# Kernel tuning notes

Measured on AMD Instinct MI355X. Metric: run time of the kernel, lower is better.

Reference implementation:

```python
import jax, jax.numpy as jnp
import numpy as np

NU, NI, E, D = 100000, 50000, 600000, 128
NEG_SLOPE = 0.2
EPS = 1e-12


def setup_inputs() -> dict:
    key = jax.random.key(0)
    ks = jax.random.split(key, 10)
    s = 1.0 / np.sqrt(D)  # xavier-ish scale for W
    return {
        "feat_user": jax.random.normal(ks[0], (NU, D), jnp.float32),
        "feat_item": jax.random.normal(ks[1], (NI, D), jnp.float32),
        "norm_user": jax.random.uniform(ks[2], (NU, 1), jnp.float32),
        "norm_item": jax.random.uniform(ks[3], (NI, 1), jnp.float32),
        "norm_ui": jax.random.uniform(ks[4], (E, 1), jnp.float32),
        "norm_iu": jax.random.uniform(ks[5], (E, 1), jnp.float32),
        "W1": jax.random.normal(ks[6], (D, D), jnp.float32) * s,
        "b1": jnp.zeros((D,), jnp.float32),
        "W2": jax.random.normal(ks[7], (D, D), jnp.float32) * s,
        "b2": jnp.zeros((D,), jnp.float32),
        "edge_u": jax.random.randint(ks[8], (E,), 0, NU),
        "edge_i": jax.random.randint(ks[9], (E,), 0, NI),
    }


def _post(h):
    # leaky_relu(0.2) -> dropout (eval: identity) -> row-wise L2 normalize
    h = jnp.where(h > 0, h, NEG_SLOPE * h)
    nrm = jnp.sqrt(jnp.sum(h * h, axis=1, keepdims=True))
    return h / jnp.maximum(nrm, EPS)


def reference(feat_user, feat_item, norm_user, norm_item, norm_ui, norm_iu,
              W1, b1, W2, b2, edge_u, edge_i):
    # edge_message = u_mul_v over ui edges of normed features  [E, D]
    edge_message = (feat_user * norm_user)[edge_u] * (feat_item * norm_item)[edge_i]

    # u_mul_e_sum(iu_g, feat_item, norm_iu): sum_e feat_item[i_e]*norm_iu[e] -> user
    agg_user = jax.ops.segment_sum(feat_item[edge_i] * norm_iu, edge_u, num_segments=NU)
    # u_mul_e_sum(ui_g, feat_user, norm_ui): sum_e feat_user[u_e]*norm_ui[e] -> item
    agg_item = jax.ops.segment_sum(feat_user[edge_u] * norm_ui, edge_i, num_segments=NI)

    # copy_e_sum of edge_message into user (iu dst) and item (ui dst)
    msg_user = jax.ops.segment_sum(edge_message, edge_u, num_segments=NU)
    msg_item = jax.ops.segment_sum(edge_message, edge_i, num_segments=NI)

    h_user = (feat_user + agg_user) @ W1.T + b1 + msg_user @ W2.T + b2
    h_item = (feat_item + agg_item) @ W1.T + b1 + msg_item @ W2.T + b2

    return _post(h_user), _post(h_item)
```

## Files before the change

kernel.cpp:

```cpp
#include <hip/hip_runtime.h>
#include <hip/hip_fp16.h>

#define NU_ 100000
#define NI_ 50000
#define E_  600000
#define DD  128
#define NT_ (NU_ + NI_)

#define BKN 64
#define NBKT ((NT_ + 63) >> 6)
#define SBLK 8192
#define NSB ((E_ + SBLK - 1) / SBLK)
#define NL (NBKT * NSB)
#define NSCB ((NL + 2047) / 2048)
#define MAXE 1024

#define TOBF_BLKS ((NT_ * DD / 8 + 511) / 512)
#define PACK_BLKS 8
#define PREP_BLKS (NSB + TOBF_BLKS + PACK_BLKS)

typedef short bf16x8 __attribute__((ext_vector_type(8)));
typedef float f32x4 __attribute__((ext_vector_type(4)));
typedef unsigned short u16x8 __attribute__((ext_vector_type(8)));

__device__ __forceinline__ unsigned short f2bf(float x) {
  unsigned u = __float_as_uint(x);
  return (unsigned short)((u + 0x7FFFu + ((u >> 16) & 1u)) >> 16);
}
__device__ __forceinline__ float bf2f(unsigned short h) {
  return __uint_as_float((unsigned)h << 16);
}

__device__ __forceinline__ int sidx(int L) {
  int bkt = L / NSB;
  int sb = L - bkt * NSB;
  return sb * NBKT + bkt;
}

__device__ __forceinline__ int swz(int nn, int b) {
  return nn * 256 + (b ^ ((nn & 7) << 4));
}
__device__ __forceinline__ int swz2(int row, int b) {
  return row * 512 + (b ^ ((row & 7) << 4));
}

__global__ __launch_bounds__(512) void prep_kernel(
    const float* __restrict__ fu, const float* __restrict__ fi,
    const float* __restrict__ W1, const float* __restrict__ W2,
    const int* __restrict__ eu, const int* __restrict__ ei,
    unsigned short* __restrict__ fub, unsigned short* __restrict__ fib,
    unsigned short* __restrict__ Bp, int* __restrict__ hist) {
  __shared__ int cnt[NBKT];
  int bid = blockIdx.x, tid = threadIdx.x;

  if (bid < NSB) {
    int sb = bid;
    for (int k = tid; k < NBKT; k += 512) cnt[k] = 0;
    __syncthreads();
#pragma unroll
    for (int j = 0; j < SBLK / 512; j++) {
      int e = sb * SBLK + j * 512 + tid;
      if (e < E_) {
        atomicAdd(&cnt[eu[e] >> 6], 1);
        atomicAdd(&cnt[(NU_ + ei[e]) >> 6], 1);
      }
    }
    __syncthreads();
    for (int k = tid; k < NBKT; k += 512) hist[sb * NBKT + k] = cnt[k];
    return;
  }

  if (bid < NSB + TOBF_BLKS) {
    int t = (bid - NSB) * 512 + tid;
    int nu8 = NU_ * DD / 8;
    int nt8 = NT_ * DD / 8;
    if (t >= nt8) return;
    const float* src;
    unsigned short* dst;
    int k;
    if (t < nu8) { src = fu; dst = fub; k = t; }
    else { src = fi; dst = fib; k = t - nu8; }
    const float4 v0 = reinterpret_cast<const float4*>(src)[k * 2];
    const float4 v1 = reinterpret_cast<const float4*>(src)[k * 2 + 1];
    u16x8 o;
    o[0] = f2bf(v0.x); o[1] = f2bf(v0.y); o[2] = f2bf(v0.z); o[3] = f2bf(v0.w);
    o[4] = f2bf(v1.x); o[5] = f2bf(v1.y); o[6] = f2bf(v1.z); o[7] = f2bf(v1.w);
    reinterpret_cast<u16x8*>(dst)[k] = o;
    return;
  }

  int t = (bid - NSB - TOBF_BLKS) * 512 + tid;
  if (t >= 4096) return;
  int w = t >> 11;
  int l = t & 63;
  int kt = (t >> 6) & 3;
  int nt = (t >> 8) & 7;
  const float* W = w ? W2 : W1;
  int n = nt * 16 + (l & 15);
  int k0 = kt * 32 + (l >> 4) * 8;
  unsigned short* dst = Bp + (size_t)t * 8;
#pragma unroll
  for (int j = 0; j < 8; j++) dst[j] = f2bf(W[n * DD + k0 + j]);
}

__global__ __launch_bounds__(256) void scanA_kernel(
    const int* __restrict__ hist, int* __restrict__ off, int* __restrict__ bsum) {
  __shared__ int ts[256];
  int tid = threadIdx.x;
  int base = blockIdx.x * 2048 + tid * 8;
  int v[8];
  int s = 0;
#pragma unroll
  for (int j = 0; j < 8; j++) {
    v[j] = s;
    int L = base + j;
    s += (L < NL) ? hist[sidx(L)] : 0;
  }
  ts[tid] = s;
  __syncthreads();
  for (int ofs = 1; ofs < 256; ofs <<= 1) {
    int add = (tid >= ofs) ? ts[tid - ofs] : 0;
    __syncthreads();
    ts[tid] += add;
    __syncthreads();
  }
  int texcl = ts[tid] - s;
#pragma unroll
  for (int j = 0; j < 8; j++) {
    int L = base + j;
    if (L < NL) off[sidx(L)] = texcl + v[j];
  }
  if (tid == 255) bsum[blockIdx.x] = ts[255];
}

__global__ void scanB_kernel(int* __restrict__ bsum) {
  if (threadIdx.x == 0) {
    int s = 0;
    for (int n = 0; n < NSCB; n++) {
      int t = bsum[n];
      bsum[n] = s;
      s += t;
    }
  }
}

__global__ __launch_bounds__(512) void scatter_kernel(
    const int* __restrict__ eu, const int* __restrict__ ei,
    const float* __restrict__ nui, const float* __restrict__ niu,
    const int* __restrict__ off, const int* __restrict__ bsum,
    int2* __restrict__ binned) {
  __shared__ int cur[NBKT];
  int sb = blockIdx.x, tid = threadIdx.x;
  for (int k = tid; k < NBKT; k += 512)
    cur[k] = off[sb * NBKT + k] + bsum[(k * NSB + sb) >> 11];
  __syncthreads();
#pragma unroll
  for (int j = 0; j < SBLK / 512; j++) {
    int e = sb * SBLK + j * 512 + tid;
    if (e < E_) {
      int u = eu[e], i = ei[e];
      int gi = NU_ + i;
      int s1 = atomicAdd(&cur[u >> 6], 1);
      binned[s1] = make_int2(((u & 63) << 20) | i, __float_as_int(niu[e]));
      int s2 = atomicAdd(&cur[gi >> 6], 1);
      binned[s2] = make_int2(((gi & 63) << 20) | u, __float_as_int(nui[e]));
    }
  }
}

__global__ __launch_bounds__(512, 8) void fused_kernel(
    const unsigned short* __restrict__ fub, const unsigned short* __restrict__ fib,
    const float* __restrict__ nu, const float* __restrict__ ni,
    const int* __restrict__ off, const int* __restrict__ bsum,
    const int2* __restrict__ binned,
    const unsigned short* __restrict__ Bp,
    const float* __restrict__ b1, const float* __restrict__ b2,
    float* __restrict__ out) {
  __shared__ __align__(16) unsigned short XM[2 * BKN * 128];
  __shared__ int eidx[MAXE];
  __shared__ unsigned short ew[MAXE];
  __shared__ int csrtmp[128];
  __shared__ int nstart[BKN + 1];

  unsigned short* Xs = XM;
  unsigned short* Ms = XM + BKN * 128;
  int* ncnt = csrtmp;
  int* ncur = csrtmp + 64;

  int bkt = blockIdx.x, tid = threadIdx.x;
  int bs = off[bkt] + bsum[(bkt * NSB) >> 11];
  int be = (bkt + 1 < NBKT) ? off[bkt + 1] + bsum[((bkt + 1) * NSB) >> 11] : 2 * E_;
  int cnt = be - bs;
  if (cnt > MAXE) cnt = MAXE;

  if (tid < BKN) ncnt[tid] = 0;
  __syncthreads();
  int2 e0, e1;
  bool h0 = tid < cnt, h1 = tid + 512 < cnt;
  if (h0) {
    e0 = binned[bs + tid];
    atomicAdd(&ncnt[(e0.x >> 20) & 63], 1);
  }
  if (h1) {
    e1 = binned[bs + tid + 512];
    atomicAdd(&ncnt[(e1.x >> 20) & 63], 1);
  }
  __syncthreads();

  if (tid < BKN) {
    int a = ncnt[tid];
    int incl = a;
#pragma unroll
    for (int ofs = 1; ofs < 64; ofs <<= 1) {
      int t = __shfl_up(incl, ofs);
      if (tid >= ofs) incl += t;
    }
    if (tid == 0) nstart[0] = 0;
    nstart[tid + 1] = incl;
    ncur[tid] = incl - a;
  }
  __syncthreads();

  if (h0) {
    int slot = atomicAdd(&ncur[(e0.x >> 20) & 63], 1);
    eidx[slot] = e0.x;
    ew[slot] = __half_as_ushort(__float2half(__int_as_float(e0.y)));
  }
  if (h1) {
    int slot = atomicAdd(&ncur[(e1.x >> 20) & 63], 1);
    eidx[slot] = e1.x;
    ew[slot] = __half_as_ushort(__float2half(__int_as_float(e1.y)));
  }
  __syncthreads();

  int wid = tid >> 6, lane = tid & 63;
  int q = lane >> 4, sub = lane & 15;

  for (int nn = 0; nn < 8; nn++) {
    int gl = wid * 8 + nn;
    int g = bkt * BKN + gl;
    if (g >= NT_) break;
    bool isU = g < NU_;
    const unsigned short* nbF = isU ? fib : fub;
    const float* nbS = isU ? ni : nu;
    int cs = nstart[gl], ce = nstart[gl + 1];

    float aA[8] = {0.f, 0.f, 0.f, 0.f, 0.f, 0.f, 0.f, 0.f};
    float aM[8] = {0.f, 0.f, 0.f, 0.f, 0.f, 0.f, 0.f, 0.f};
    for (int j = cs + q; j < ce; j += 4) {
      int idx = eidx[j] & 0xFFFFF;
      float w = __half2float(__ushort_as_half(ew[j]));
      float snb = nbS[idx];
      u16x8 f = *reinterpret_cast<const u16x8*>(nbF + (size_t)idx * DD + sub * 8);
#pragma unroll
      for (int d = 0; d < 8; d++) {
        float r = bf2f((unsigned short)f[d]);
        aA[d] += r * w;
        aM[d] += r * snb;
      }
    }
#pragma unroll
    for (int d = 0; d < 8; d++) {
      aA[d] += __shfl_xor(aA[d], 16);
      aA[d] += __shfl_xor(aA[d], 32);
      aM[d] += __shfl_xor(aM[d], 16);
      aM[d] += __shfl_xor(aM[d], 32);
    }

    int lrow = isU ? g : g - NU_;
    if (q < 2) {
      const unsigned short* ownp = (isU ? fub : fib) + (size_t)lrow * DD + sub * 8;
      u16x8 fo = *reinterpret_cast<const u16x8*>(ownp);
      u16x8 o;
      if (q == 0) {
#pragma unroll
        for (int d = 0; d < 8; d++)
          o[d] = f2bf(bf2f((unsigned short)fo[d]) + aA[d]);
        *reinterpret_cast<u16x8*>((char*)Xs + swz(gl, sub * 16)) = o;
      } else {
        float so = isU ? nu[lrow] : ni[lrow];
#pragma unroll
        for (int d = 0; d < 8; d++)
          o[d] = f2bf(bf2f((unsigned short)fo[d]) * so * aM[d]);
        *reinterpret_cast<u16x8*>((char*)Ms + swz(gl, sub * 16)) = o;
      }
    }
  }
  __syncthreads();

  int t = wid >> 1, colHalf = wid & 1;
  int gt0 = bkt * BKN + t * 16;
  bool active = gt0 < NT_;

  int lm = lane & 15, lh = lane >> 4;
  float h[4][4];
  float inv4[4];
  float (*ssx)[2] = (float(*)[2])csrtmp;

  if (active) {
    f32x4 acc[4];
#pragma unroll
    for (int nt = 0; nt < 4; nt++) acc[nt] = (f32x4){0.f, 0.f, 0.f, 0.f};

#pragma unroll
    for (int kt = 0; kt < 4; kt++) {
      int b = kt * 64 + lh * 16;
      bf16x8 a1 = *reinterpret_cast<const bf16x8*>((char*)Xs + swz(t * 16 + lm, b));
      bf16x8 a2 = *reinterpret_cast<const bf16x8*>((char*)Ms + swz(t * 16 + lm, b));
#pragma unroll
      for (int nt = 0; nt < 4; nt++) {
        int ntp = colHalf * 4 + nt;
        bf16x8 bf1 = *reinterpret_cast<const bf16x8*>(Bp + ((size_t)((0 * 8 + ntp) * 4 + kt) * 64 + lane) * 8);
        acc[nt] = __builtin_amdgcn_mfma_f32_16x16x32_bf16(a1, bf1, acc[nt], 0, 0, 0);
        bf16x8 bf2 = *reinterpret_cast<const bf16x8*>(Bp + ((size_t)((1 * 8 + ntp) * 4 + kt) * 64 + lane) * 8);
        acc[nt] = __builtin_amdgcn_mfma_f32_16x16x32_bf16(a2, bf2, acc[nt], 0, 0, 0);
      }
    }

    float ss[4] = {0.f, 0.f, 0.f, 0.f};
#pragma unroll
    for (int nt = 0; nt < 4; nt++) {
      int ntp = colHalf * 4 + nt;
      float bb = b1[ntp * 16 + lm] + b2[ntp * 16 + lm];
#pragma unroll
      for (int r = 0; r < 4; r++) {
        float v = acc[nt][r] + bb;
        v = (v > 0.f) ? v : 0.2f * v;
        h[nt][r] = v;
        ss[r] += v * v;
      }
    }
#pragma unroll
    for (int r = 0; r < 4; r++) {
#pragma unroll
      for (int m = 1; m < 16; m <<= 1) ss[r] += __shfl_xor(ss[r], m);
    }
    if (lm == 0) {
#pragma unroll
      for (int r = 0; r < 4; r++) ssx[t * 16 + lh * 4 + r][colHalf] = ss[r];
    }
  }
  __syncthreads();

  if (active) {
#pragma unroll
    for (int r = 0; r < 4; r++) {
      int row = t * 16 + lh * 4 + r;
      float tot = ssx[row][0] + ssx[row][1];
      inv4[r] = 1.0f / fmaxf(sqrtf(tot), 1e-12f);
    }
    float* stg = reinterpret_cast<float*>(XM);
#pragma unroll
    for (int nt = 0; nt < 4; nt++) {
      int ntp = colHalf * 4 + nt;
#pragma unroll
      for (int r = 0; r < 4; r++) {
        int row = t * 16 + lh * 4 + r;
        *reinterpret_cast<float*>((char*)stg + swz2(row, ntp * 64 + lm * 4)) =
            h[nt][r] * inv4[r];
      }
    }
  }
  __syncthreads();

  float* stg = reinterpret_cast<float*>(XM);
  int maxrow = NT_ - bkt * BKN;
  float* ob = out + (size_t)bkt * BKN * DD;
#pragma unroll
  for (int k = 0; k < 4; k++) {
    int c = k * 512 + tid;
    int row = c >> 5;
    if (row < maxrow) {
      f32x4 v = *reinterpret_cast<const f32x4*>((char*)stg + swz2(row, (c & 31) * 16));
      *reinterpret_cast<f32x4*>(ob + (size_t)c * 4) = v;
    }
  }
}

extern "C" void kernel_launch(void* const* d_in, const int* in_sizes, int n_in,
                              void* d_out, int out_size, void* d_ws, size_t ws_size,
                              hipStream_t stream) {
  const float* fu  = (const float*)d_in[0];
  const float* fi  = (const float*)d_in[1];
  const float* nu  = (const float*)d_in[2];
  const float* ni  = (const float*)d_in[3];
  const float* nui = (const float*)d_in[4];
  const float* niu = (const float*)d_in[5];
  const float* W1  = (const float*)d_in[6];
  const float* b1  = (const float*)d_in[7];
  const float* W2  = (const float*)d_in[8];
  const float* b2  = (const float*)d_in[9];
  const int* eu    = (const int*)d_in[10];
  const int* ei    = (const int*)d_in[11];
  float* out = (float*)d_out;
  char* ws = (char*)d_ws;

  size_t off_b = 0;
  auto alloc = [&](size_t bytes) {
    char* p = ws + off_b;
    off_b += (bytes + 255) & ~(size_t)255;
    return p;
  };
  unsigned short* fub = (unsigned short*)alloc((size_t)NU_ * DD * 2);
  unsigned short* fib = (unsigned short*)alloc((size_t)NI_ * DD * 2);
  unsigned short* Bp  = (unsigned short*)alloc(4096 * 8 * 2);
  int* hist = (int*)alloc((size_t)NL * 4);
  int* offc = (int*)alloc((size_t)NL * 4);
  int* bsum = (int*)alloc(256 * 4);
  int2* binned = (int2*)alloc((size_t)2 * E_ * 8);

  prep_kernel<<<PREP_BLKS, 512, 0, stream>>>(fu, fi, W1, W2, eu, ei,
                                             fub, fib, Bp, hist);
  scanA_kernel<<<NSCB, 256, 0, stream>>>(hist, offc, bsum);
  scanB_kernel<<<1, 64, 0, stream>>>(bsum);
  scatter_kernel<<<NSB, 512, 0, stream>>>(eu, ei, nui, niu, offc, bsum, binned);

  fused_kernel<<<NBKT, 512, 0, stream>>>(
      fub, fib, nu, ni, offc, bsum, binned, Bp, b1, b2, out);
}
```

Before: 166.1 us.

## Replace per-superblock histogram scan with global bucket counts and atomic cursor scatter

The binning pipeline changes from a full superblock-by-bucket histogram with a two-level scan to global bucket counts built with atomics. A single-block scan then produces bucket offsets, and the scatter claims per-block ranges through atomic global cursors. This drops one kernel launch and the large histogram traffic, and the bf16 feature conversion moves into the scatter launch. The gather loop in the fused kernel is also unrolled by two with packed float2 bf16 unpacking. Ordering of edges within a bucket becomes nondeterministic, which changes summation order.

```diff
diff --git a/kernel.cpp b/kernel.cpp
--- a/kernel.cpp
+++ b/kernel.cpp
@@ -11,16 +11,14 @@
 #define NBKT ((NT_ + 63) >> 6)
 #define SBLK 8192
 #define NSB ((E_ + SBLK - 1) / SBLK)
-#define NL (NBKT * NSB)
-#define NSCB ((NL + 2047) / 2048)
 #define MAXE 1024
 
 #define TOBF_BLKS ((NT_ * DD / 8 + 511) / 512)
 #define PACK_BLKS 8
-#define PREP_BLKS (NSB + TOBF_BLKS + PACK_BLKS)
 
 typedef short bf16x8 __attribute__((ext_vector_type(8)));
 typedef float f32x4 __attribute__((ext_vector_type(4)));
+typedef float f32x2 __attribute__((ext_vector_type(2)));
 typedef unsigned short u16x8 __attribute__((ext_vector_type(8)));
 
 __device__ __forceinline__ unsigned short f2bf(float x) {
@@ -31,12 +29,6 @@
   return __uint_as_float((unsigned)h << 16);
 }
 
-__device__ __forceinline__ int sidx(int L) {
-  int bkt = L / NSB;
-  int sb = L - bkt * NSB;
-  return sb * NBKT + bkt;
-}
-
 __device__ __forceinline__ int swz(int nn, int b) {
   return nn * 256 + (b ^ ((nn & 7) << 4));
 }
@@ -45,51 +37,33 @@
 }
 
 __global__ __launch_bounds__(512) void prep_kernel(
-    const float* __restrict__ fu, const float* __restrict__ fi,
+    const int* __restrict__ eu, const int* __restrict__ ei,
     const float* __restrict__ W1, const float* __restrict__ W2,
-    const int* __restrict__ eu, const int* __restrict__ ei,
-    unsigned short* __restrict__ fub, unsigned short* __restrict__ fib,
-    unsigned short* __restrict__ Bp, int* __restrict__ hist) {
-  __shared__ int cnt[NBKT];
+    unsigned short* __restrict__ Bp, int* __restrict__ cnt) {
+  __shared__ int loc[NBKT];
   int bid = blockIdx.x, tid = threadIdx.x;
 
   if (bid < NSB) {
     int sb = bid;
-    for (int k = tid; k < NBKT; k += 512) cnt[k] = 0;
+    for (int k = tid; k < NBKT; k += 512) loc[k] = 0;
     __syncthreads();
 #pragma unroll
     for (int j = 0; j < SBLK / 512; j++) {
       int e = sb * SBLK + j * 512 + tid;
       if (e < E_) {
-        atomicAdd(&cnt[eu[e] >> 6], 1);
-        atomicAdd(&cnt[(NU_ + ei[e]) >> 6], 1);
-      }
-    }
-    __syncthreads();
-    for (int k = tid; k < NBKT; k += 512) hist[sb * NBKT + k] = cnt[k];
+        atomicAdd(&loc[eu[e] >> 6], 1);
+        atomicAdd(&loc[(NU_ + ei[e]) >> 6], 1);
+      }
+    }
+    __syncthreads();
+    for (int k = tid; k < NBKT; k += 512) {
+      int c = loc[k];
+      if (c) atomicAdd(&cnt[k], c);
+    }
     return;
   }
 
-  if (bid < NSB + TOBF_BLKS) {
-    int t = (bid - NSB) * 512 + tid;
-    int nu8 = NU_ * DD / 8;
-    int nt8 = NT_ * DD / 8;
-    if (t >= nt8) return;
-    const float* src;
-    unsigned short* dst;
-    int k;
-    if (t < nu8) { src = fu; dst = fub; k = t; }
-    else { src = fi; dst = fib; k = t - nu8; }
-    const float4 v0 = reinterpret_cast<const float4*>(src)[k * 2];
-    const float4 v1 = reinterpret_cast<const float4*>(src)[k * 2 + 1];
-    u16x8 o;
-    o[0] = f2bf(v0.x); o[1] = f2bf(v0.y); o[2] = f2bf(v0.z); o[3] = f2bf(v0.w);
-    o[4] = f2bf(v1.x); o[5] = f2bf(v1.y); o[6] = f2bf(v1.z); o[7] = f2bf(v1.w);
-    reinterpret_cast<u16x8*>(dst)[k] = o;
-    return;
-  }
-
-  int t = (bid - NSB - TOBF_BLKS) * 512 + tid;
+  int t = (bid - NSB) * 512 + tid;
   if (t >= 4096) return;
   int w = t >> 11;
   int l = t & 63;
@@ -103,22 +77,22 @@
   for (int j = 0; j < 8; j++) dst[j] = f2bf(W[n * DD + k0 + j]);
 }
 
-__global__ __launch_bounds__(256) void scanA_kernel(
-    const int* __restrict__ hist, int* __restrict__ off, int* __restrict__ bsum) {
-  __shared__ int ts[256];
+__global__ __launch_bounds__(1024) void bscan_kernel(
+    const int* __restrict__ cnt, int* __restrict__ boff, int* __restrict__ gcur) {
+  __shared__ int ts[1024];
   int tid = threadIdx.x;
-  int base = blockIdx.x * 2048 + tid * 8;
-  int v[8];
+  int base = tid * 3;
+  int v[3];
   int s = 0;
 #pragma unroll
-  for (int j = 0; j < 8; j++) {
+  for (int j = 0; j < 3; j++) {
     v[j] = s;
-    int L = base + j;
-    s += (L < NL) ? hist[sidx(L)] : 0;
+    int k = base + j;
+    s += (k < NBKT) ? cnt[k] : 0;
   }
   ts[tid] = s;
   __syncthreads();
-  for (int ofs = 1; ofs < 256; ofs <<= 1) {
+  for (int ofs = 1; ofs < 1024; ofs <<= 1) {
     int add = (tid >= ofs) ? ts[tid - ofs] : 0;
     __syncthreads();
     ts[tid] += add;
@@ -126,53 +100,80 @@
   }
   int texcl = ts[tid] - s;
 #pragma unroll
-  for (int j = 0; j < 8; j++) {
-    int L = base + j;
-    if (L < NL) off[sidx(L)] = texcl + v[j];
-  }
-  if (tid == 255) bsum[blockIdx.x] = ts[255];
-}
-
-__global__ void scanB_kernel(int* __restrict__ bsum) {
-  if (threadIdx.x == 0) {
-    int s = 0;
-    for (int n = 0; n < NSCB; n++) {
-      int t = bsum[n];
-      bsum[n] = s;
-      s += t;
-    }
-  }
-}
-
-__global__ __launch_bounds__(512) void scatter_kernel(
+  for (int j = 0; j < 3; j++) {
+    int k = base + j;
+    if (k < NBKT) {
+      int o = texcl + v[j];
+      boff[k] = o;
+      gcur[k] = o;
+    }
+  }
+  if (tid == 1023) boff[NBKT] = ts[1023];
+}
+
+__global__ __launch_bounds__(512) void sct_kernel(
     const int* __restrict__ eu, const int* __restrict__ ei,
     const float* __restrict__ nui, const float* __restrict__ niu,
-    const int* __restrict__ off, const int* __restrict__ bsum,
-    int2* __restrict__ binned) {
-  __shared__ int cur[NBKT];
-  int sb = blockIdx.x, tid = threadIdx.x;
-  for (int k = tid; k < NBKT; k += 512)
-    cur[k] = off[sb * NBKT + k] + bsum[(k * NSB + sb) >> 11];
-  __syncthreads();
-#pragma unroll
-  for (int j = 0; j < SBLK / 512; j++) {
-    int e = sb * SBLK + j * 512 + tid;
-    if (e < E_) {
-      int u = eu[e], i = ei[e];
-      int gi = NU_ + i;
-      int s1 = atomicAdd(&cur[u >> 6], 1);
-      binned[s1] = make_int2(((u & 63) << 20) | i, __float_as_int(niu[e]));
-      int s2 = atomicAdd(&cur[gi >> 6], 1);
-      binned[s2] = make_int2(((gi & 63) << 20) | u, __float_as_int(nui[e]));
-    }
-  }
+    const float* __restrict__ fu, const float* __restrict__ fi,
+    unsigned short* __restrict__ fub, unsigned short* __restrict__ fib,
+    int* __restrict__ gcur, int2* __restrict__ binned) {
+  __shared__ int loc[NBKT];
+  int bid = blockIdx.x, tid = threadIdx.x;
+
+  if (bid < NSB) {
+    int sb = bid;
+    for (int k = tid; k < NBKT; k += 512) loc[k] = 0;
+    __syncthreads();
+#pragma unroll
+    for (int j = 0; j < SBLK / 512; j++) {
+      int e = sb * SBLK + j * 512 + tid;
+      if (e < E_) {
+        atomicAdd(&loc[eu[e] >> 6], 1);
+        atomicAdd(&loc[(NU_ + ei[e]) >> 6], 1);
+      }
+    }
+    __syncthreads();
+    for (int k = tid; k < NBKT; k += 512) {
+      int c = loc[k];
+      loc[k] = c ? atomicAdd(&gcur[k], c) : 0;
+    }
+    __syncthreads();
+#pragma unroll
+    for (int j = 0; j < SBLK / 512; j++) {
+      int e = sb * SBLK + j * 512 + tid;
+      if (e < E_) {
+        int u = eu[e], i = ei[e];
+        int gi = NU_ + i;
+        int s1 = atomicAdd(&loc[u >> 6], 1);
+        binned[s1] = make_int2(((u & 63) << 20) | i, __float_as_int(niu[e]));
+        int s2 = atomicAdd(&loc[gi >> 6], 1);
+        binned[s2] = make_int2(((gi & 63) << 20) | u, __float_as_int(nui[e]));
+      }
+    }
+    return;
+  }
+
+  int t = (bid - NSB) * 512 + tid;
+  int nu8 = NU_ * DD / 8;
+  int nt8 = NT_ * DD / 8;
+  if (t >= nt8) return;
+  const float* src;
+  unsigned short* dst;
+  int k;
+  if (t < nu8) { src = fu; dst = fub; k = t; }
+  else { src = fi; dst = fib; k = t - nu8; }
+  const float4 v0 = reinterpret_cast<const float4*>(src)[k * 2];
+  const float4 v1 = reinterpret_cast<const float4*>(src)[k * 2 + 1];
+  u16x8 o;
+  o[0] = f2bf(v0.x); o[1] = f2bf(v0.y); o[2] = f2bf(v0.z); o[3] = f2bf(v0.w);
+  o[4] = f2bf(v1.x); o[5] = f2bf(v1.y); o[6] = f2bf(v1.z); o[7] = f2bf(v1.w);
+  reinterpret_cast<u16x8*>(dst)[k] = o;
 }
 
 __global__ __launch_bounds__(512, 8) void fused_kernel(
     const unsigned short* __restrict__ fub, const unsigned short* __restrict__ fib,
     const float* __restrict__ nu, const float* __restrict__ ni,
-    const int* __restrict__ off, const int* __restrict__ bsum,
-    const int2* __restrict__ binned,
+    const int* __restrict__ boff, const int2* __restrict__ binned,
     const unsigned short* __restrict__ Bp,
     const float* __restrict__ b1, const float* __restrict__ b2,
     float* __restrict__ out) {
@@ -188,8 +189,8 @@
   int* ncur = csrtmp + 64;
 
   int bkt = blockIdx.x, tid = threadIdx.x;
-  int bs = off[bkt] + bsum[(bkt * NSB) >> 11];
-  int be = (bkt + 1 < NBKT) ? off[bkt + 1] + bsum[((bkt + 1) * NSB) >> 11] : 2 * E_;
+  int bs = boff[bkt];
+  int be = boff[bkt + 1];
   int cnt = be - bs;
   if (cnt > MAXE) cnt = MAXE;
 
@@ -223,12 +224,12 @@
 
   if (h0) {
     int slot = atomicAdd(&ncur[(e0.x >> 20) & 63], 1);
-    eidx[slot] = e0.x;
+    eidx[slot] = e0.x & 0xFFFFF;
     ew[slot] = __half_as_ushort(__float2half(__int_as_float(e0.y)));
   }
   if (h1) {
     int slot = atomicAdd(&ncur[(e1.x >> 20) & 63], 1);
-    eidx[slot] = e1.x;
+    eidx[slot] = e1.x & 0xFFFFF;
     ew[slot] = __half_as_ushort(__float2half(__int_as_float(e1.y)));
   }
   __syncthreads();
@@ -245,26 +246,59 @@
     const float* nbS = isU ? ni : nu;
     int cs = nstart[gl], ce = nstart[gl + 1];
 
-    float aA[8] = {0.f, 0.f, 0.f, 0.f, 0.f, 0.f, 0.f, 0.f};
-    float aM[8] = {0.f, 0.f, 0.f, 0.f, 0.f, 0.f, 0.f, 0.f};
-    for (int j = cs + q; j < ce; j += 4) {
-      int idx = eidx[j] & 0xFFFFF;
-      float w = __half2float(__ushort_as_half(ew[j]));
-      float snb = nbS[idx];
-      u16x8 f = *reinterpret_cast<const u16x8*>(nbF + (size_t)idx * DD + sub * 8);
-#pragma unroll
-      for (int d = 0; d < 8; d++) {
-        float r = bf2f((unsigned short)f[d]);
-        aA[d] += r * w;
-        aM[d] += r * snb;
-      }
-    }
-#pragma unroll
-    for (int d = 0; d < 8; d++) {
-      aA[d] += __shfl_xor(aA[d], 16);
-      aA[d] += __shfl_xor(aA[d], 32);
-      aM[d] += __shfl_xor(aM[d], 16);
-      aM[d] += __shfl_xor(aM[d], 32);
+    f32x2 pA[4], pM[4];
+#pragma unroll
+    for (int k = 0; k < 4; k++) {
+      pA[k] = (f32x2){0.f, 0.f};
+      pM[k] = (f32x2){0.f, 0.f};
+    }
+
+#define GPAIRS(dd, wv, sv)                                                   \
+    {                                                                        \
+      f32x2 r0, r1, r2, r3;                                                  \
+      r0.x = __uint_as_float((dd).x << 16);                                  \
+      r0.y = __uint_as_float((dd).x & 0xFFFF0000u);                          \
+      r1.x = __uint_as_float((dd).y << 16);                                  \
+      r1.y = __uint_as_float((dd).y & 0xFFFF0000u);                          \
+      r2.x = __uint_as_float((dd).z << 16);                                  \
+      r2.y = __uint_as_float((dd).z & 0xFFFF0000u);                          \
+      r3.x = __uint_as_float((dd).w << 16);                                  \
+      r3.y = __uint_as_float((dd).w & 0xFFFF0000u);                          \
+      pA[0] += r0 * (wv); pM[0] += r0 * (sv);                                \
+      pA[1] += r1 * (wv); pM[1] += r1 * (sv);                                \
+      pA[2] += r2 * (wv); pM[2] += r2 * (sv);                                \
+      pA[3] += r3 * (wv); pM[3] += r3 * (sv);                                \
+    }
+
+    int j = cs + q;
+    for (; j + 4 < ce; j += 8) {
+      int i0 = eidx[j], i1 = eidx[j + 4];
+      float w0 = __half2float(__ushort_as_half(ew[j]));
+      float w1 = __half2float(__ushort_as_half(ew[j + 4]));
+      float s0 = nbS[i0], s1 = nbS[i1];
+      uint4 d0 = *reinterpret_cast<const uint4*>(nbF + (size_t)i0 * DD + sub * 8);
+      uint4 d1 = *reinterpret_cast<const uint4*>(nbF + (size_t)i1 * DD + sub * 8);
+      f32x2 wv0 = {w0, w0}, sv0 = {s0, s0};
+      f32x2 wv1 = {w1, w1}, sv1 = {s1, s1};
+      GPAIRS(d0, wv0, sv0);
+      GPAIRS(d1, wv1, sv1);
+    }
+    if (j < ce) {
+      int i0 = eidx[j];
+      float w0 = __half2float(__ushort_as_half(ew[j]));
+      float s0 = nbS[i0];
+      uint4 d0 = *reinterpret_cast<const uint4*>(nbF + (size_t)i0 * DD + sub * 8);
+      f32x2 wv0 = {w0, w0}, sv0 = {s0, s0};
+      GPAIRS(d0, wv0, sv0);
+    }
+#undef GPAIRS
+
+#pragma unroll
+    for (int k = 0; k < 4; k++) {
+      pA[k].x += __shfl_xor(pA[k].x, 16); pA[k].x += __shfl_xor(pA[k].x, 32);
+      pA[k].y += __shfl_xor(pA[k].y, 16); pA[k].y += __shfl_xor(pA[k].y, 32);
+      pM[k].x += __shfl_xor(pM[k].x, 16); pM[k].x += __shfl_xor(pM[k].x, 32);
+      pM[k].y += __shfl_xor(pM[k].y, 16); pM[k].y += __shfl_xor(pM[k].y, 32);
     }
 
     int lrow = isU ? g : g - NU_;
@@ -274,14 +308,18 @@
       u16x8 o;
       if (q == 0) {
 #pragma unroll
-        for (int d = 0; d < 8; d++)
-          o[d] = f2bf(bf2f((unsigned short)fo[d]) + aA[d]);
+        for (int k = 0; k < 4; k++) {
+          o[2 * k] = f2bf(bf2f((unsigned short)fo[2 * k]) + pA[k].x);
+          o[2 * k + 1] = f2bf(bf2f((unsigned short)fo[2 * k + 1]) + pA[k].y);
+        }
         *reinterpret_cast<u16x8*>((char*)Xs + swz(gl, sub * 16)) = o;
       } else {
         float so = isU ? nu[lrow] : ni[lrow];
 #pragma unroll
-        for (int d = 0; d < 8; d++)
-          o[d] = f2bf(bf2f((unsigned short)fo[d]) * so * aM[d]);
+        for (int k = 0; k < 4; k++) {
+          o[2 * k] = f2bf(bf2f((unsigned short)fo[2 * k]) * so * pM[k].x);
+          o[2 * k + 1] = f2bf(bf2f((unsigned short)fo[2 * k + 1]) * so * pM[k].y);
+        }
         *reinterpret_cast<u16x8*>((char*)Ms + swz(gl, sub * 16)) = o;
       }
     }
@@ -404,17 +442,18 @@
   unsigned short* fub = (unsigned short*)alloc((size_t)NU_ * DD * 2);
   unsigned short* fib = (unsigned short*)alloc((size_t)NI_ * DD * 2);
   unsigned short* Bp  = (unsigned short*)alloc(4096 * 8 * 2);
-  int* hist = (int*)alloc((size_t)NL * 4);
-  int* offc = (int*)alloc((size_t)NL * 4);
-  int* bsum = (int*)alloc(256 * 4);
+  int* cnt  = (int*)alloc(NBKT * 4);
+  int* boff = (int*)alloc((NBKT + 1) * 4);
+  int* gcur = (int*)alloc(NBKT * 4);
   int2* binned = (int2*)alloc((size_t)2 * E_ * 8);
 
-  prep_kernel<<<PREP_BLKS, 512, 0, stream>>>(fu, fi, W1, W2, eu, ei,
-                                             fub, fib, Bp, hist);
-  scanA_kernel<<<NSCB, 256, 0, stream>>>(hist, offc, bsum);
-  scanB_kernel<<<1, 64, 0, stream>>>(bsum);
-  scatter_kernel<<<NSB, 512, 0, stream>>>(eu, ei, nui, niu, offc, bsum, binned);
+  hipMemsetAsync(cnt, 0, NBKT * sizeof(int), stream);
+
+  prep_kernel<<<NSB + PACK_BLKS, 512, 0, stream>>>(eu, ei, W1, W2, Bp, cnt);
+  bscan_kernel<<<1, 1024, 0, stream>>>(cnt, boff, gcur);
+  sct_kernel<<<NSB + TOBF_BLKS, 512, 0, stream>>>(
+      eu, ei, nui, niu, fu, fi, fub, fib, gcur, binned);
 
   fused_kernel<<<NBKT, 512, 0, stream>>>(
-      fub, fib, nu, ni, offc, bsum, binned, Bp, b1, b2, out);
-}
+      fub, fib, nu, ni, boff, binned, Bp, b1, b2, out);
+}
```

Result: slower. 173.7 us (+4.6%).
